# Optimization experiments

Measured on AMD Instinct MI355X. Metric: run time of the kernel, lower is better.

Reference implementation:

```python
import jax, jax.numpy as jnp
import numpy as np

NUM_HEADS = 16
FUTURE_FRAMES = 2
DIM = 1024


def setup_inputs() -> dict:
    key = jax.random.key(0)
    kx, kqkv, kp, kb = jax.random.split(key, 4)
    B, T = 2, 2048
    x = jax.random.normal(kx, (B, T, DIM), dtype=jnp.float32)
    # torch Linear weights stored transposed for direct x @ W use
    w_qkv = jax.random.normal(kqkv, (DIM, 3 * DIM), dtype=jnp.float32) * (DIM ** -0.5)
    w_proj = jax.random.normal(kp, (DIM, DIM), dtype=jnp.float32) * (DIM ** -0.5)
    b_proj = jax.random.normal(kb, (DIM,), dtype=jnp.float32) * 0.01
    return {"x": x, "w_qkv": w_qkv, "w_proj": w_proj, "b_proj": b_proj}


def reference(x, w_qkv, w_proj, b_proj):
    B, T, dim = x.shape
    H = NUM_HEADS
    hd = dim // H
    qkv = x @ w_qkv                                    # (B, T, 3*dim)
    q, k, v = jnp.split(qkv, 3, axis=-1)
    # (B, H, T, hd)
    q = q.reshape(B, T, H, hd).transpose(0, 2, 1, 3)
    k = k.reshape(B, T, H, hd).transpose(0, 2, 1, 3)
    v = v.reshape(B, T, H, hd).transpose(0, 2, 1, 3)
    scale = hd ** -0.5
    scores = jnp.einsum('bhqd,bhkd->bhqk', q, k) * scale
    # banded mask: query i may attend keys j with i <= j <= i + future_frames
    i = jnp.arange(T)[:, None]
    j = jnp.arange(T)[None, :]
    allowed = (j >= i) & (j <= i + FUTURE_FRAMES)       # (T, T)
    scores = jnp.where(allowed[None, None], scores, -jnp.inf)
    attn = jax.nn.softmax(scores, axis=-1)
    out = jnp.einsum('bhqk,bhkd->bhqd', attn, v)        # (B, H, T, hd)
    out = out.transpose(0, 2, 1, 3).reshape(B, T, dim)
    return out @ w_proj + b_proj
```

## Files before the change

kernel.cpp:

```cpp
#include <hip/hip_runtime.h>
#include <hip/hip_bf16.h>
#include <cstdint>
#include <cstddef>

#define T_SEQ 2048
#define NBATCH 2
#define DIMSZ 1024
#define NHEAD 16
#define HDIM 64

typedef float f32x4 __attribute__((ext_vector_type(4)));
typedef short bf16x8 __attribute__((ext_vector_type(8)));

__device__ __forceinline__ void gld_lds16(const __hip_bfloat16* g, __hip_bfloat16* l) {
    __builtin_amdgcn_global_load_lds(
        (const __attribute__((address_space(1))) unsigned int*)g,
        (__attribute__((address_space(3))) unsigned int*)l,
        16, 0, 0);
}

__device__ __forceinline__ float bf2f(unsigned short u) {
    union { unsigned int i; float f; } c; c.i = (unsigned int)u << 16; return c.f;
}

__global__ __launch_bounds__(256) void prep(
    const float* __restrict__ x,      __hip_bfloat16* __restrict__ xb,
    const float* __restrict__ wqkv,   __hip_bfloat16* __restrict__ wqkvT,
    const float* __restrict__ wproj,  __hip_bfloat16* __restrict__ wprojT)
{
    __shared__ float tile[32][33];
    const int b = blockIdx.x;
    if (b < 4096) {
        int i = (b * 256 + threadIdx.x) * 4;
        float4 v = *(const float4*)(x + i);
        union { __hip_bfloat16 h[4]; ushort4 u; } pk;
        pk.h[0] = __hip_bfloat16(v.x); pk.h[1] = __hip_bfloat16(v.y);
        pk.h[2] = __hip_bfloat16(v.z); pk.h[3] = __hip_bfloat16(v.w);
        *(ushort4*)(xb + i) = pk.u;
        return;
    }
    const float* in; __hip_bfloat16* out; int C, c0, r0;
    if (b < 7168) {
        int bb = b - 4096; in = wqkv; out = wqkvT; C = 3072;
        c0 = (bb % 96) * 32; r0 = (bb / 96) * 32;
    } else {
        int bb = b - 7168; in = wproj; out = wprojT; C = 1024;
        c0 = (bb & 31) * 32; r0 = (bb >> 5) * 32;
    }
    const int tx = threadIdx.x & 31, ty = threadIdx.x >> 5;
#pragma unroll
    for (int p = 0; p < 32; p += 8)
        tile[ty + p][tx] = in[(size_t)(r0 + ty + p) * C + c0 + tx];
    __syncthreads();
#pragma unroll
    for (int p = 0; p < 32; p += 8)
        out[(size_t)(c0 + ty + p) * 1024 + r0 + tx] = __hip_bfloat16(tile[tx][ty + p]);
}

__global__ __launch_bounds__(256) void gemm_bt_128(
    const __hip_bfloat16* __restrict__ A,
    const __hip_bfloat16* __restrict__ Bt,
    __hip_bfloat16* __restrict__ C,
    int M, int N, int K)
{
    __shared__ __align__(16) __hip_bfloat16 As[2 * 128 * 32];
    __shared__ __align__(16) __hip_bfloat16 Bs[2 * 128 * 32];

    const int tid  = threadIdx.x;
    const int wv   = tid >> 6;
    const int lane = tid & 63;
    const int bn   = blockIdx.x, bm = blockIdx.y;
    const int wm   = wv >> 1, wn = wv & 1;

    f32x4 acc[4][4] = {};

    const int srow = lane >> 2;
    const int scol = (lane & 3) * 8;

    const __hip_bfloat16* Ag = A  + (size_t)(bm * 128) * K;
    const __hip_bfloat16* Bg = Bt + (size_t)(bn * 128) * K;

    const int fm = lane & 15;
    const int fq = (lane >> 4) * 8;

    for (int kk = 0; kk < K; kk += 64) {
#pragma unroll
        for (int kh = 0; kh < 2; ++kh)
#pragma unroll
            for (int it = 0; it < 2; ++it) {
                int row = (it * 4 + wv) * 16 + srow;
                gld_lds16(Ag + (size_t)row * K + kk + kh * 32 + scol,
                          As + kh * 4096 + row * 32 + scol);
                gld_lds16(Bg + (size_t)row * K + kk + kh * 32 + scol,
                          Bs + kh * 4096 + row * 32 + scol);
            }
        __syncthreads();

#pragma unroll
        for (int kh = 0; kh < 2; ++kh) {
            bf16x8 af[4], bfr[4];
#pragma unroll
            for (int i = 0; i < 4; ++i)
                af[i] = *(const bf16x8*)(As + kh * 4096 + (wm * 64 + i * 16 + fm) * 32 + fq);
#pragma unroll
            for (int j = 0; j < 4; ++j)
                bfr[j] = *(const bf16x8*)(Bs + kh * 4096 + (wn * 64 + j * 16 + fm) * 32 + fq);
#pragma unroll
            for (int i = 0; i < 4; ++i)
#pragma unroll
                for (int j = 0; j < 4; ++j)
                    acc[i][j] = __builtin_amdgcn_mfma_f32_16x16x32_bf16(af[i], bfr[j], acc[i][j], 0, 0, 0);
        }
        __syncthreads();
    }

    const int fcol  = lane & 15;
    const int frow4 = (lane >> 4) * 4;
    const int cm0 = bm * 128 + wm * 64;
    const int cn0 = bn * 128 + wn * 64;
#pragma unroll
    for (int j = 0; j < 4; ++j) {
        int col = cn0 + j * 16 + fcol;
#pragma unroll
        for (int i = 0; i < 4; ++i)
#pragma unroll
            for (int r = 0; r < 4; ++r) {
                int row = cm0 + i * 16 + frow4 + r;
                C[(size_t)row * N + col] = __hip_bfloat16(acc[i][j][r]);
            }
    }
}

__global__ __launch_bounds__(256) void gemm_bt_64(
    const __hip_bfloat16* __restrict__ A,
    const __hip_bfloat16* __restrict__ Bt,
    const float* __restrict__ bias,
    float* __restrict__ C,
    int M, int N, int K)
{
    __shared__ __align__(16) __hip_bfloat16 As[2 * 64 * 32];
    __shared__ __align__(16) __hip_bfloat16 Bs[2 * 128 * 32];

    const int tid  = threadIdx.x;
    const int wv   = tid >> 6;
    const int lane = tid & 63;
    const int bn   = blockIdx.x, bm = blockIdx.y;
    const int wm   = wv >> 1, wn = wv & 1;

    f32x4 acc[2][4] = {};

    const int srow = lane >> 2;
    const int scol = (lane & 3) * 8;

    const __hip_bfloat16* Ag = A  + (size_t)(bm * 64) * K;
    const __hip_bfloat16* Bg = Bt + (size_t)(bn * 128) * K;

    const int fm = lane & 15;
    const int fq = (lane >> 4) * 8;

    for (int kk = 0; kk < K; kk += 64) {
#pragma unroll
        for (int kh = 0; kh < 2; ++kh) {
            {
                int row = wv * 16 + srow;
                gld_lds16(Ag + (size_t)row * K + kk + kh * 32 + scol,
                          As + kh * 2048 + row * 32 + scol);
            }
#pragma unroll
            for (int it = 0; it < 2; ++it) {
                int row = (it * 4 + wv) * 16 + srow;
                gld_lds16(Bg + (size_t)row * K + kk + kh * 32 + scol,
                          Bs + kh * 4096 + row * 32 + scol);
            }
        }
        __syncthreads();

#pragma unroll
        for (int kh = 0; kh < 2; ++kh) {
            bf16x8 af[2], bfr[4];
#pragma unroll
            for (int i = 0; i < 2; ++i)
                af[i] = *(const bf16x8*)(As + kh * 2048 + (wm * 32 + i * 16 + fm) * 32 + fq);
#pragma unroll
            for (int j = 0; j < 4; ++j)
                bfr[j] = *(const bf16x8*)(Bs + kh * 4096 + (wn * 64 + j * 16 + fm) * 32 + fq);
#pragma unroll
            for (int i = 0; i < 2; ++i)
#pragma unroll
                for (int j = 0; j < 4; ++j)
                    acc[i][j] = __builtin_amdgcn_mfma_f32_16x16x32_bf16(af[i], bfr[j], acc[i][j], 0, 0, 0);
        }
        __syncthreads();
    }

    const int fcol  = lane & 15;
    const int frow4 = (lane >> 4) * 4;
    const int cm0 = bm * 64 + wm * 32;
    const int cn0 = bn * 128 + wn * 64;
#pragma unroll
    for (int j = 0; j < 4; ++j) {
        int col = cn0 + j * 16 + fcol;
        float bv = bias[col];
#pragma unroll
        for (int i = 0; i < 2; ++i)
#pragma unroll
            for (int r = 0; r < 4; ++r) {
                int row = cm0 + i * 16 + frow4 + r;
                C[(size_t)row * N + col] = acc[i][j][r] + bv;
            }
    }
}

__global__ __launch_bounds__(256) void attn_banded(
    const __hip_bfloat16* __restrict__ qkv,
    __hip_bfloat16* __restrict__ o)
{
    const int t4 = threadIdx.x;
    const int r  = blockIdx.x;
    const int t  = r & (T_SEQ - 1);
    const size_t rb = (size_t)r * (3 * DIMSZ);
    const int d0 = t4 * 4;

    ushort4 qu = *(const ushort4*)(qkv + rb + d0);
    float q0 = bf2f(qu.x), q1 = bf2f(qu.y), q2 = bf2f(qu.z), q3 = bf2f(qu.w);

    float s[3], vvx[3], vvy[3], vvz[3], vvw[3];
#pragma unroll
    for (int j = 0; j < 3; ++j) {
        bool ok = (t + j) < T_SEQ;
        size_t rbj = ok ? rb + (size_t)j * (3 * DIMSZ) : rb;
        ushort4 ku = *(const ushort4*)(qkv + rbj + DIMSZ + d0);
        ushort4 vu = *(const ushort4*)(qkv + rbj + 2 * DIMSZ + d0);
        vvx[j] = bf2f(vu.x); vvy[j] = bf2f(vu.y); vvz[j] = bf2f(vu.z); vvw[j] = bf2f(vu.w);
        float d = q0 * bf2f(ku.x) + q1 * bf2f(ku.y) + q2 * bf2f(ku.z) + q3 * bf2f(ku.w);
#pragma unroll
        for (int off = 8; off > 0; off >>= 1)
            d += __shfl_xor(d, off, 64);
        s[j] = ok ? d * 0.125f : -1e30f;
    }
    float m  = fmaxf(s[0], fmaxf(s[1], s[2]));
    float p0 = __expf(s[0] - m), p1 = __expf(s[1] - m), p2 = __expf(s[2] - m);
    float inv = 1.0f / (p0 + p1 + p2);
    union { __hip_bfloat16 h[4]; ushort4 uu; } pk;
    pk.h[0] = __hip_bfloat16((p0 * vvx[0] + p1 * vvx[1] + p2 * vvx[2]) * inv);
    pk.h[1] = __hip_bfloat16((p0 * vvy[0] + p1 * vvy[1] + p2 * vvy[2]) * inv);
    pk.h[2] = __hip_bfloat16((p0 * vvz[0] + p1 * vvz[1] + p2 * vvz[2]) * inv);
    pk.h[3] = __hip_bfloat16((p0 * vvw[0] + p1 * vvw[1] + p2 * vvw[2]) * inv);
    *(ushort4*)(o + (size_t)r * DIMSZ + d0) = pk.uu;
}

extern "C" void kernel_launch(void* const* d_in, const int* in_sizes, int n_in,
                              void* d_out, int out_size, void* d_ws, size_t ws_size,
                              hipStream_t stream) {
    const float* x      = (const float*)d_in[0];
    const float* w_qkv  = (const float*)d_in[1];
    const float* w_proj = (const float*)d_in[2];
    const float* b_proj = (const float*)d_in[3];
    float* out = (float*)d_out;

    const int M = NBATCH * T_SEQ;

    char* ws = (char*)d_ws;
    __hip_bfloat16* xb     = (__hip_bfloat16*)(ws);
    __hip_bfloat16* attn   = (__hip_bfloat16*)(ws);
    __hip_bfloat16* wqkvT  = (__hip_bfloat16*)(ws + (8u  << 20));
    __hip_bfloat16* wprojT = (__hip_bfloat16*)(ws + (14u << 20));
    __hip_bfloat16* qkv    = (__hip_bfloat16*)(ws + (16u << 20));

    prep<<<8192, 256, 0, stream>>>(x, xb, w_qkv, wqkvT, w_proj, wprojT);

    gemm_bt_128<<<dim3(3 * DIMSZ / 128, M / 128), 256, 0, stream>>>(
        xb, wqkvT, qkv, M, 3 * DIMSZ, DIMSZ);

    attn_banded<<<M, 256, 0, stream>>>(qkv, attn);

    gemm_bt_64<<<dim3(DIMSZ / 128, M / 64), 256, 0, stream>>>(
        attn, wprojT, b_proj, out, M, DIMSZ, DIMSZ);
}
```

Baseline: 143.7 us.

## Replace QKV GEMM with 256x256 tile, 4-stage LDS ring pipeline kernel

Replaces the 128x128 double-buffered QKV projection GEMM with a 256x256-tile, 512-thread kernel that uses a 4-slot LDS ring and prefetches three k-tiles ahead, gated by s_waitcnt vmcnt. It adds an XOR swizzle on LDS columns to reduce bank conflicts, an XCD-aware block-index remap, and setprio and sched_barrier around the MFMA block. The goal is to raise reuse per loaded tile and overlap global loads with compute. In exchange it needs 128 KB of LDS per block and many accumulator registers. The grid shrinks to 192 blocks, which may leave some CUs idle.

```diff
diff --git a/kernel.cpp b/kernel.cpp
--- a/kernel.cpp
+++ b/kernel.cpp
@@ -57,76 +57,110 @@
         out[(size_t)(c0 + ty + p) * 1024 + r0 + tx] = __hip_bfloat16(tile[tx][ty + p]);
 }
 
-__global__ __launch_bounds__(256) void gemm_bt_128(
+#define BAR() do { asm volatile("" ::: "memory"); __builtin_amdgcn_s_barrier(); \
+                   asm volatile("" ::: "memory"); } while (0)
+
+#define STAGE1(G, S, rb, kt)                                                   \
+    do {                                                                       \
+        _Pragma("unroll")                                                      \
+        for (int s_ = 0; s_ < 2; ++s_) {                                       \
+            int row_ = s_ * 128 + (tid >> 2);                                  \
+            int cbg_ = scb ^ (((row_ >> 1) & 3) << 4);                        \
+            gld_lds16(G + (size_t)row_ * K + (kt) * 32 + (cbg_ >> 1),          \
+                      &S[rb][row_ * 32 + (scb >> 1)]);                         \
+        }                                                                      \
+    } while (0)
+
+__global__ __launch_bounds__(512, 2) void gemm256_ring(
     const __hip_bfloat16* __restrict__ A,
     const __hip_bfloat16* __restrict__ Bt,
     __hip_bfloat16* __restrict__ C,
     int M, int N, int K)
 {
-    __shared__ __align__(16) __hip_bfloat16 As[2 * 128 * 32];
-    __shared__ __align__(16) __hip_bfloat16 Bs[2 * 128 * 32];
+    __shared__ __align__(16) __hip_bfloat16 As[4][256 * 32];
+    __shared__ __align__(16) __hip_bfloat16 Bs[4][256 * 32];
 
     const int tid  = threadIdx.x;
+    const int lane = tid & 63;
     const int wv   = tid >> 6;
-    const int lane = tid & 63;
-    const int bn   = blockIdx.x, bm = blockIdx.y;
-    const int wm   = wv >> 1, wn = wv & 1;
-
-    f32x4 acc[4][4] = {};
-
-    const int srow = lane >> 2;
-    const int scol = (lane & 3) * 8;
-
-    const __hip_bfloat16* Ag = A  + (size_t)(bm * 128) * K;
-    const __hip_bfloat16* Bg = Bt + (size_t)(bn * 128) * K;
+    const int wm   = wv >> 2;
+    const int wn   = wv & 3;
+
+    const int nwg = gridDim.x;
+    const int cpx = nwg >> 3;
+    const int bid = blockIdx.x;
+    const int swb = (bid & 7) * cpx + (bid >> 3);
+    const int nbn = N >> 8;
+    const int bm = swb / nbn, bn = swb % nbn;
+
+    const int NT = K >> 5;
+
+    const __hip_bfloat16* Ag = A  + (size_t)(bm << 8) * K;
+    const __hip_bfloat16* Bg = Bt + (size_t)(bn << 8) * K;
+
+    const int scb = (tid & 3) << 4;
 
     const int fm = lane & 15;
-    const int fq = (lane >> 4) * 8;
-
-    for (int kk = 0; kk < K; kk += 64) {
-#pragma unroll
-        for (int kh = 0; kh < 2; ++kh)
-#pragma unroll
-            for (int it = 0; it < 2; ++it) {
-                int row = (it * 4 + wv) * 16 + srow;
-                gld_lds16(Ag + (size_t)row * K + kk + kh * 32 + scol,
-                          As + kh * 4096 + row * 32 + scol);
-                gld_lds16(Bg + (size_t)row * K + kk + kh * 32 + scol,
-                          Bs + kh * 4096 + row * 32 + scol);
-            }
-        __syncthreads();
-
-#pragma unroll
-        for (int kh = 0; kh < 2; ++kh) {
-            bf16x8 af[4], bfr[4];
-#pragma unroll
-            for (int i = 0; i < 4; ++i)
-                af[i] = *(const bf16x8*)(As + kh * 4096 + (wm * 64 + i * 16 + fm) * 32 + fq);
+    const int fq = (lane >> 4) << 3;
+
+    f32x4 acc[8][4] = {};
+
+    STAGE1(Ag, As, 0, 0); STAGE1(Bg, Bs, 0, 0);
+    STAGE1(Ag, As, 1, 1); STAGE1(Bg, Bs, 1, 1);
+    STAGE1(Ag, As, 2, 2); STAGE1(Bg, Bs, 2, 2);
+
+    for (int s = 0; s < NT; ++s) {
+        int kt3 = s + 3; if (kt3 >= NT) kt3 -= NT;
+        const int rcur = s & 3;
+        const int rnxt = kt3 & 3;
+
+        STAGE1(Ag, As, rnxt, kt3);
+        STAGE1(Bg, Bs, rnxt, kt3);
+
+        asm volatile("s_waitcnt vmcnt(12)" ::: "memory");
+        BAR();
+
+        bf16x8 af[8], bfv[4];
+#pragma unroll
+        for (int i = 0; i < 8; ++i) {
+            int row_ = wm * 128 + i * 16 + fm;
+            int ce_  = fq ^ (((row_ >> 1) & 3) << 3);
+            af[i] = *(const bf16x8*)&As[rcur][row_ * 32 + ce_];
+        }
+#pragma unroll
+        for (int j = 0; j < 4; ++j) {
+            int row_ = wn * 64 + j * 16 + fm;
+            int ce_  = fq ^ (((row_ >> 1) & 3) << 3);
+            bfv[j] = *(const bf16x8*)&Bs[rcur][row_ * 32 + ce_];
+        }
+
+        __builtin_amdgcn_sched_barrier(0);
+        __builtin_amdgcn_s_setprio(1);
+#pragma unroll
+        for (int i = 0; i < 8; ++i)
 #pragma unroll
             for (int j = 0; j < 4; ++j)
-                bfr[j] = *(const bf16x8*)(Bs + kh * 4096 + (wn * 64 + j * 16 + fm) * 32 + fq);
-#pragma unroll
-            for (int i = 0; i < 4; ++i)
-#pragma unroll
-                for (int j = 0; j < 4; ++j)
-                    acc[i][j] = __builtin_amdgcn_mfma_f32_16x16x32_bf16(af[i], bfr[j], acc[i][j], 0, 0, 0);
-        }
-        __syncthreads();
-    }
+                acc[i][j] = __builtin_amdgcn_mfma_f32_16x16x32_bf16(
+                    af[i], bfv[j], acc[i][j], 0, 0, 0);
+        __builtin_amdgcn_s_setprio(0);
+        __builtin_amdgcn_sched_barrier(0);
+        BAR();
+    }
+    asm volatile("s_waitcnt vmcnt(0)" ::: "memory");
 
     const int fcol  = lane & 15;
-    const int frow4 = (lane >> 4) * 4;
-    const int cm0 = bm * 128 + wm * 64;
-    const int cn0 = bn * 128 + wn * 64;
-#pragma unroll
-    for (int j = 0; j < 4; ++j) {
-        int col = cn0 + j * 16 + fcol;
-#pragma unroll
-        for (int i = 0; i < 4; ++i)
+    const int frow4 = (lane >> 4) << 2;
+    const int cm0 = (bm << 8) + wm * 128;
+    const int cn0 = (bn << 8) + wn * 64;
+#pragma unroll
+    for (int nj = 0; nj < 4; ++nj) {
+        int col = cn0 + nj * 16 + fcol;
+#pragma unroll
+        for (int mi = 0; mi < 8; ++mi)
 #pragma unroll
             for (int r = 0; r < 4; ++r) {
-                int row = cm0 + i * 16 + frow4 + r;
-                C[(size_t)row * N + col] = __hip_bfloat16(acc[i][j][r]);
+                int row = cm0 + mi * 16 + frow4 + r;
+                C[(size_t)row * N + col] = __hip_bfloat16(acc[mi][nj][r]);
             }
     }
 }
@@ -138,8 +172,8 @@
     float* __restrict__ C,
     int M, int N, int K)
 {
-    __shared__ __align__(16) __hip_bfloat16 As[2 * 64 * 32];
-    __shared__ __align__(16) __hip_bfloat16 Bs[2 * 128 * 32];
+    __shared__ __align__(16) __hip_bfloat16 As2[2 * 64 * 32];
+    __shared__ __align__(16) __hip_bfloat16 Bs2[2 * 128 * 32];
 
     const int tid  = threadIdx.x;
     const int wv   = tid >> 6;
@@ -164,13 +198,13 @@
             {
                 int row = wv * 16 + srow;
                 gld_lds16(Ag + (size_t)row * K + kk + kh * 32 + scol,
-                          As + kh * 2048 + row * 32 + scol);
+                          As2 + kh * 2048 + row * 32 + scol);
             }
 #pragma unroll
             for (int it = 0; it < 2; ++it) {
                 int row = (it * 4 + wv) * 16 + srow;
                 gld_lds16(Bg + (size_t)row * K + kk + kh * 32 + scol,
-                          Bs + kh * 4096 + row * 32 + scol);
+                          Bs2 + kh * 4096 + row * 32 + scol);
             }
         }
         __syncthreads();
@@ -180,10 +214,10 @@
             bf16x8 af[2], bfr[4];
 #pragma unroll
             for (int i = 0; i < 2; ++i)
-                af[i] = *(const bf16x8*)(As + kh * 2048 + (wm * 32 + i * 16 + fm) * 32 + fq);
+                af[i] = *(const bf16x8*)(As2 + kh * 2048 + (wm * 32 + i * 16 + fm) * 32 + fq);
 #pragma unroll
             for (int j = 0; j < 4; ++j)
-                bfr[j] = *(const bf16x8*)(Bs + kh * 4096 + (wn * 64 + j * 16 + fm) * 32 + fq);
+                bfr[j] = *(const bf16x8*)(Bs2 + kh * 4096 + (wn * 64 + j * 16 + fm) * 32 + fq);
 #pragma unroll
             for (int i = 0; i < 2; ++i)
 #pragma unroll
@@ -269,7 +303,7 @@
 
     prep<<<8192, 256, 0, stream>>>(x, xb, w_qkv, wqkvT, w_proj, wprojT);
 
-    gemm_bt_128<<<dim3(3 * DIMSZ / 128, M / 128), 256, 0, stream>>>(
+    gemm256_ring<<<dim3((M / 256) * (3 * DIMSZ / 256)), 512, 0, stream>>>(
         xb, wqkvT, qkv, M, 3 * DIMSZ, DIMSZ);
 
     attn_banded<<<M, 256, 0, stream>>>(qkv, attn);
```

Result: slower. 157.4 us (+9.6%).
